# Kernel tuning notes

Hardware: AMD Instinct MI355X
Metric: run time of the kernel (lower is better)

Reference implementation:

```python
import jax, jax.numpy as jnp
import numpy as np

N_HEAD = 16
D_MODEL = 1024
D_K = D_MODEL // N_HEAD  # 64
NEG = -1000000000.0


def setup_inputs() -> dict:
    key = jax.random.key(0)
    ks = jax.random.split(key, 7)
    B, L = 4, 2048
    q = jax.random.normal(ks[0], (B, L, D_MODEL), dtype=jnp.float32)
    k = jax.random.normal(ks[1], (B, L, D_MODEL), dtype=jnp.float32)
    v = jax.random.normal(ks[2], (B, L, D_MODEL), dtype=jnp.float32)
    mask = jnp.ones((B, L, L), dtype=jnp.int32)
    s = 1.0 / np.sqrt(D_MODEL)
    w_q = jax.random.normal(ks[3], (D_MODEL, D_MODEL), dtype=jnp.float32) * s
    w_k = jax.random.normal(ks[4], (D_MODEL, D_MODEL), dtype=jnp.float32) * s
    w_v = jax.random.normal(ks[5], (D_MODEL, D_MODEL), dtype=jnp.float32) * s
    w_o = jax.random.normal(ks[6], (D_MODEL, D_MODEL), dtype=jnp.float32) * s
    return {"q": q, "k": k, "v": v, "w_q": w_q, "w_k": w_k, "w_v": w_v, "w_o": w_o, "mask": mask}


def reference(q, k, v, w_q, w_k, w_v, w_o, mask):
    B, Lq, _ = q.shape
    temperature = jnp.asarray(D_K, q.dtype) ** 0.5
    # Projections (Linear, no bias): x @ W^T, then split heads -> [B, H, L, d_k]
    qh = (q @ w_q.T).reshape(B, Lq, N_HEAD, D_K).transpose(0, 2, 1, 3)
    kh = (k @ w_k.T).reshape(B, -1, N_HEAD, D_K).transpose(0, 2, 1, 3)
    vh = (v @ w_v.T).reshape(B, -1, N_HEAD, D_K).transpose(0, 2, 1, 3)
    # Scaled dot-product attention, full [B, H, Lq, Lk] scores materialized
    attn = jnp.einsum("bhqd,bhkd->bhqk", qh / temperature, kh)
    attn = jnp.where(mask[:, None, :, :] == 0, NEG, attn)
    attn = jax.nn.softmax(attn, axis=-1)  # dropout is identity in eval mode
    out = jnp.einsum("bhqk,bhkd->bhqd", attn, vh)
    out = out.transpose(0, 2, 1, 3).reshape(B, Lq, D_MODEL)
    return out @ w_o.T
```

## Files before the change

### kernel.cpp

```cpp
#include <hip/hip_runtime.h>
#include <stdint.h>

typedef float  f32x4  __attribute__((ext_vector_type(4)));
typedef __bf16 bf16x8 __attribute__((ext_vector_type(8)));
typedef short  s16x8  __attribute__((ext_vector_type(8)));
typedef short  s16x4  __attribute__((ext_vector_type(4)));
typedef unsigned int   u32;
typedef unsigned short u16;
typedef u32 u32x2 __attribute__((ext_vector_type(2)));
typedef u32 u32x4 __attribute__((ext_vector_type(4)));

#define DM 1024
#define LQ 2048
#define NH 16

__device__ __forceinline__ u16 f2bf(float f) {
    unsigned int u = __builtin_bit_cast(unsigned int, f);
    u += 0x7FFFu + ((u >> 16) & 1u);
    return (u16)(u >> 16);
}

__device__ __forceinline__ float fexp2(float x) {
#if __has_builtin(__builtin_amdgcn_exp2f)
    return __builtin_amdgcn_exp2f(x);
#else
    return exp2f(x);
#endif
}

__device__ __forceinline__ u32 cvtpk(float lo, float hi) {
    u32 r;
    asm("v_cvt_pk_bf16_f32 %0, %1, %2" : "=v"(r) : "v"(lo), "v"(hi));
    return r;
}

__device__ __forceinline__ float max3f(float a, float b, float c) {
    float r;
    asm("v_max3_f32 %0, %1, %2, %3" : "=v"(r) : "v"(a), "v"(b), "v"(c));
    return r;
}

__device__ __forceinline__ u32 permb(u32 b, u32 a, u32 sel) {
    u32 r;
    asm("v_perm_b32 %0, %1, %2, %3" : "=v"(r) : "v"(b), "v"(a), "s"(sel));
    return r;
}

__device__ __forceinline__ f32x4 mfma32(s16x8 a, s16x8 b, f32x4 c) {
    return __builtin_amdgcn_mfma_f32_16x16x32_bf16(
        __builtin_bit_cast(bf16x8, a), __builtin_bit_cast(bf16x8, b), c, 0, 0, 0);
}

#define GLD16(gp, lp) __builtin_amdgcn_global_load_lds( \
    (__attribute__((address_space(1))) void*)(gp),      \
    (__attribute__((address_space(3))) void*)(lp), 16, 0, 0)

__global__ void k_mask_check(const int4* __restrict__ m4, int n4, int* flag) {
    bool z = false;
    for (int i = blockIdx.x * blockDim.x + threadIdx.x; i < n4;
         i += gridDim.x * blockDim.x) {
        int4 v = m4[i];
        if (v.x == 0 || v.y == 0 || v.z == 0 || v.w == 0) z = true;
    }
    if (__ballot(z)) {
        if ((threadIdx.x & 63) == 0) atomicAnd(flag, 0);
    }
}

__global__ void k_cvt_all(const float4* __restrict__ q,  const float4* __restrict__ k,
                          const float4* __restrict__ v,  const float4* __restrict__ wq,
                          const float4* __restrict__ wk, const float4* __restrict__ wv,
                          const float4* __restrict__ wo,
                          uint64_t* xq, uint64_t* xk, uint64_t* xv,
                          uint64_t* bwq, uint64_t* bwk, uint64_t* bwv, uint64_t* bwo,
                          int* flag)
{
    if (blockIdx.x == 0 && threadIdx.x == 0) *flag = 1;
    const int NX = 2097152, NW = 262144;
    const int total = 3 * NX + 4 * NW;
    const int stride = gridDim.x * blockDim.x;
    for (int idx = blockIdx.x * blockDim.x + threadIdx.x; idx < total; idx += stride) {
        const float4* s; uint64_t* d; int off;
        if (idx < 3 * NX) {
            int ji = idx >> 21;
            off = idx & (NX - 1);
            s = ji == 0 ? q : ji == 1 ? k : v;
            d = ji == 0 ? xq : ji == 1 ? xk : xv;
        } else {
            int r = idx - 3 * NX;
            int ji = r >> 18;
            off = r & (NW - 1);
            s = ji == 0 ? wq : ji == 1 ? wk : ji == 2 ? wv : wo;
            d = ji == 0 ? bwq : ji == 1 ? bwk : ji == 2 ? bwv : bwo;
        }
        float4 f = s[off];
        union { u16 u[4]; uint64_t qq; } rr;
        rr.u[0] = f2bf(f.x); rr.u[1] = f2bf(f.y);
        rr.u[2] = f2bf(f.z); rr.u[3] = f2bf(f.w);
        d[off] = rr.qq;
    }
}

template <int MODE>
__global__ __launch_bounds__(256) void k_gemm(
    const u16* __restrict__ A0, const u16* __restrict__ Bw0,
    u16* __restrict__ Cb0, float* __restrict__ Cf, float scale)
{
    constexpr int K = 1024;
    __shared__ char lA[128 * 32 * 2];
    __shared__ char lB[128 * 32 * 2];
    const int t = threadIdx.x, l = t & 63, w = t >> 6;
    const int q = l & 15, g = l >> 4;
    const int z = (MODE == 0) ? blockIdx.z : 0;
    const u16* A  = A0  + (size_t)z * 8388608;
    const u16* Bw = Bw0 + (size_t)z * 1048576;
    u16* Cb = (MODE == 0) ? Cb0 + (size_t)z * 8388608 : nullptr;
    const float scl = (MODE == 0 && z != 0) ? 1.0f : scale;
    const int lin = blockIdx.x;
    const int ytile = ((lin & 7) << 3) | ((lin >> 3) & 7);
    const int xtile = lin >> 6;
    const int m0 = ytile * 128, n0 = xtile * 128;
    const int wr = (w >> 1) * 64, wc = (w & 1) * 64;

    f32x4 acc[4][4];
#pragma unroll
    for (int i = 0; i < 4; i++)
#pragma unroll
        for (int j = 0; j < 4; j++) acc[i][j] = (f32x4){0.f, 0.f, 0.f, 0.f};

    for (int k0 = 0; k0 < K; k0 += 32) {
#pragma unroll
        for (int c = 0; c < 2; c++) {
            int i = c * 256 + t;
            int row = i >> 2, sl = i & 3;
            int ss = sl ^ (row & 3);
            GLD16(A  + (size_t)(m0 + row) * K + k0 + ss * 8, lA + (i - l) * 16);
            GLD16(Bw + (size_t)(n0 + row) * K + k0 + ss * 8, lB + (i - l) * 16);
        }
        __syncthreads();
        s16x8 af[4], bfr[4];
#pragma unroll
        for (int mt = 0; mt < 4; mt++) {
            int r = wr + mt * 16 + q;
            af[mt] = *(const s16x8*)(lA + r * 64 + ((g ^ (r & 3)) * 16));
        }
#pragma unroll
        for (int nt = 0; nt < 4; nt++) {
            int r = wc + nt * 16 + q;
            bfr[nt] = *(const s16x8*)(lB + r * 64 + ((g ^ (r & 3)) * 16));
        }
#pragma unroll
        for (int mt = 0; mt < 4; mt++)
#pragma unroll
            for (int nt = 0; nt < 4; nt++)
                acc[mt][nt] = mfma32(bfr[nt], af[mt], acc[mt][nt]);
        __syncthreads();
    }

#pragma unroll
    for (int mt = 0; mt < 4; mt++) {
        int m = m0 + wr + mt * 16 + q;
#pragma unroll
        for (int nt = 0; nt < 4; nt++) {
            int n = n0 + wc + nt * 16 + g * 4;
            f32x4 a = acc[mt][nt];
            if (MODE == 0) {
                int bb = m >> 11, row = m & 2047;
                int h = n >> 6, d = n & 63;
                s16x4 pk;
#pragma unroll
                for (int j = 0; j < 4; j++) pk[j] = (short)f2bf(a[j] * scl);
                *(s16x4*)(Cb + (((size_t)(bb * NH + h) * LQ + row) << 6) + d) = pk;
            } else {
                f32x4 o;
#pragma unroll
                for (int j = 0; j < 4; j++) o[j] = a[j] * scl;
                *(f32x4*)(Cf + (size_t)m * DM + n) = o;
            }
        }
    }
}

__global__ __launch_bounds__(256, 2) void k_attn(
    const u16* __restrict__ Qh, const u16* __restrict__ Kh,
    const u16* __restrict__ Vh, u16* __restrict__ ctx,
    const int* __restrict__ mask, const int* __restrict__ flag)
{
    __shared__ char lds[32768];
    char* lK0 = lds;
    char* lV0 = lds + 16384;
    const int t = threadIdx.x, l = t & 63, w = t >> 6;
    const int g = l >> 4, q = l & 15;
    const int p = blockIdx.x;
    const int bh = (p & 7) * 8 + ((p >> 3) >> 3);
    const int qt = ((p >> 3) & 7) * 256;
    const int allones = *flag;
    const size_t base = (size_t)bh * LQ * 64;
    const int dg = (l & 7) | ((w & 2) << 2);
    const int kg = (l >> 3) | ((w & 1) << 3);

    s16x8 qf[4][2];
#pragma unroll
    for (int qh = 0; qh < 4; qh++)
#pragma unroll
        for (int kh = 0; kh < 2; kh++)
            qf[qh][kh] = *(const s16x8*)(
                Qh + base + (size_t)(qt + w * 64 + qh * 16 + q) * 64 + kh * 32 + g * 8);

    f32x4 oacc[4][4];
#pragma unroll
    for (int qh = 0; qh < 4; qh++)
#pragma unroll
        for (int dt = 0; dt < 4; dt++) oacc[qh][dt] = (f32x4){0.f, 0.f, 0.f, 0.f};
    float mrow[4] = {-1e30f, -1e30f, -1e30f, -1e30f};
    float lrow[4] = {0.f, 0.f, 0.f, 0.f};

    auto stageK = [&](int kt, int b) {
#pragma unroll
        for (int c = 0; c < 2; c++) {
            int i = c * 256 + t;
            int row = i >> 3, sl = i & 7;
            GLD16(Kh + base + (size_t)(kt + row) * 64 + ((sl ^ (row & 7)) * 8),
                  lK0 + b * 8192 + (i - l) * 16);
        }
    };
    auto loadV = [&](int kt, s16x4* vr) {
#pragma unroll
        for (int j = 0; j < 4; j++)
            vr[j] = *(const s16x4*)(Vh + base + (size_t)(kt + kg * 4 + j) * 64 + dg * 4);
    };
    auto writeV = [&](const s16x4* vr, int b) {
        const u32 selLO = 0x05040100u, selHI = 0x07060302u;
        const int u = ((kg & 8) >> 1) | (kg & 3);
        const int bb2 = (kg >> 2) & 1;
        u32x2 vv[4];
#pragma unroll
        for (int j = 0; j < 4; j++) vv[j] = __builtin_bit_cast(u32x2, vr[j]);
#pragma unroll
        for (int jj = 0; jj < 4; jj++) {
            int d = dg * 4 + jj;
            u32 a0 = vv[0][jj >> 1], a1 = vv[1][jj >> 1];
            u32 a2 = vv[2][jj >> 1], a3 = vv[3][jj >> 1];
            u32 sel = (jj & 1) ? selHI : selLO;
            u32x2 pw = {permb(a1, a0, sel), permb(a3, a2, sel)};
            *(s16x4*)(lV0 + b * 8192 + d * 128 + ((u ^ (d & 7)) * 16) + bb2 * 8) =
                __builtin_bit_cast(s16x4, pw);
        }
    };

    {
        s16x4 vr[4];
        stageK(0, 0);
        loadV(0, vr);
        writeV(vr, 0);
    }

    int cur = 0;
    for (int kt = 0; kt < LQ; kt += 64) {
        __syncthreads();
        const bool more = (kt + 64) < LQ;
        s16x4 vr[4];
        if (more) {
            stageK(kt + 64, cur ^ 1);
            loadV(kt + 64, vr);
        }

        f32x4 sc[4][4];
#pragma unroll
        for (int qh = 0; qh < 4; qh++)
#pragma unroll
            for (int ct = 0; ct < 4; ct++) sc[qh][ct] = (f32x4){0.f, 0.f, 0.f, 0.f};
        __builtin_amdgcn_s_setprio(1);
#pragma unroll
        for (int ct = 0; ct < 4; ct++) {
            int kc = ct * 16 + q;
#pragma unroll
            for (int kh = 0; kh < 2; kh++) {
                s16x8 kf = *(const s16x8*)(lK0 + cur * 8192 + kc * 128 +
                                           (((kh * 4 + g) ^ (kc & 7)) * 16));
#pragma unroll
                for (int qh = 0; qh < 4; qh++)
                    sc[qh][ct] = mfma32(kf, qf[qh][kh], sc[qh][ct]);
            }
        }
        __builtin_amdgcn_s_setprio(0);

        if (!allones) {
            int b = bh >> 4;
#pragma unroll
            for (int qh = 0; qh < 4; qh++)
#pragma unroll
                for (int ct = 0; ct < 4; ct++)
#pragma unroll
                    for (int r = 0; r < 4; r++) {
                        int qr = qt + w * 64 + qh * 16 + q;
                        int kc = kt + ct * 16 + g * 4 + r;
                        if (mask[(size_t)(b * LQ + qr) * LQ + kc] == 0)
                            sc[qh][ct][r] = -1e9f;
                    }
        }

        float pm[4];
#pragma unroll
        for (int qh = 0; qh < 4; qh++) {
            float m0 = max3f(sc[qh][0][0], sc[qh][0][1], sc[qh][0][2]);
            m0 = max3f(m0, sc[qh][0][3], sc[qh][1][0]);
            m0 = max3f(m0, sc[qh][1][1], sc[qh][1][2]);
            m0 = max3f(m0, sc[qh][1][3], sc[qh][2][0]);
            m0 = max3f(m0, sc[qh][2][1], sc[qh][2][2]);
            m0 = max3f(m0, sc[qh][2][3], sc[qh][3][0]);
            m0 = max3f(m0, sc[qh][3][1], sc[qh][3][2]);
            m0 = fmaxf(m0, sc[qh][3][3]);
            m0 = fmaxf(m0, __shfl_xor(m0, 16, 64));
            m0 = fmaxf(m0, __shfl_xor(m0, 32, 64));
            pm[qh] = m0;
        }
        bool ok = pm[0] <= mrow[0] + 8.f;
        ok = ok && (pm[1] <= mrow[1] + 8.f);
        ok = ok && (pm[2] <= mrow[2] + 8.f);
        ok = ok && (pm[3] <= mrow[3] + 8.f);
        if (!__all(ok)) {
#pragma unroll
            for (int qh = 0; qh < 4; qh++) {
                float nm = fmaxf(mrow[qh], pm[qh]);
                float corr = fexp2(mrow[qh] - nm);
                mrow[qh] = nm;
                lrow[qh] *= corr;
                float cv[4];
#pragma unroll
                for (int r = 0; r < 4; r++) cv[r] = __shfl(corr, g * 4 + r, 64);
#pragma unroll
                for (int dt = 0; dt < 4; dt++)
#pragma unroll
                    for (int r = 0; r < 4; r++) oacc[qh][dt][r] *= cv[r];
            }
        }
        s16x8 pa32[4][2];
#pragma unroll
        for (int qh = 0; qh < 4; qh++) {
            float rs = 0.f;
#pragma unroll
            for (int ct = 0; ct < 4; ct++)
#pragma unroll
                for (int r = 0; r < 4; r++) {
                    float e = fexp2(sc[qh][ct][r] - mrow[qh]);
                    sc[qh][ct][r] = e;
                    rs += e;
                }
            rs += __shfl_xor(rs, 16, 64);
            rs += __shfl_xor(rs, 32, 64);
            lrow[qh] += rs;
#pragma unroll
            for (int s = 0; s < 2; s++) {
                u32x4 pv;
                pv.x = cvtpk(sc[qh][2 * s][0],     sc[qh][2 * s][1]);
                pv.y = cvtpk(sc[qh][2 * s][2],     sc[qh][2 * s][3]);
                pv.z = cvtpk(sc[qh][2 * s + 1][0], sc[qh][2 * s + 1][1]);
                pv.w = cvtpk(sc[qh][2 * s + 1][2], sc[qh][2 * s + 1][3]);
                pa32[qh][s] = __builtin_bit_cast(s16x8, pv);
            }
        }

        __builtin_amdgcn_s_setprio(1);
#pragma unroll
        for (int dt = 0; dt < 4; dt++) {
#pragma unroll
            for (int s = 0; s < 2; s++) {
                s16x8 vf = *(const s16x8*)(lV0 + cur * 8192 + (dt * 16 + q) * 128 +
                                           (((4 * s + g) ^ (q & 7)) * 16));
#pragma unroll
                for (int qh = 0; qh < 4; qh++)
                    oacc[qh][dt] = mfma32(pa32[qh][s], vf, oacc[qh][dt]);
            }
        }
        __builtin_amdgcn_s_setprio(0);

        if (more) writeV(vr, cur ^ 1);
        cur ^= 1;
    }

    __syncthreads();
    char* eb = lds + w * 8192;
#pragma unroll
    for (int qh = 0; qh < 4; qh++) {
        float lv[4];
#pragma unroll
        for (int r = 0; r < 4; r++) lv[r] = 1.f / __shfl(lrow[qh], g * 4 + r, 64);
#pragma unroll
        for (int dt = 0; dt < 4; dt++)
#pragma unroll
            for (int r = 0; r < 4; r++) {
                int row = qh * 16 + g * 4 + r;
                int cb = ((dt * 16 + q) * 2) ^ ((row & 7) << 4);
                *(u16*)(eb + row * 128 + cb) = f2bf(oacc[qh][dt][r] * lv[r]);
            }
    }
    __syncthreads();
    const int b = bh >> 4, h = bh & 15;
    const int token = qt + w * 64 + l;
    u16* gp = ctx + (size_t)(b * LQ + token) * DM + h * 64;
#pragma unroll
    for (int j = 0; j < 8; j++) {
        int cb = (j * 16) ^ ((l & 7) << 4);
        *(s16x8*)(gp + j * 8) = *(const s16x8*)(eb + l * 128 + cb);
    }
}

extern "C" void kernel_launch(void* const* d_in, const int* in_sizes, int n_in,
                              void* d_out, int out_size, void* d_ws, size_t ws_size,
                              hipStream_t stream)
{
    const float* q  = (const float*)d_in[0];
    const float* k  = (const float*)d_in[1];
    const float* v  = (const float*)d_in[2];
    const float* wq = (const float*)d_in[3];
    const float* wk = (const float*)d_in[4];
    const float* wv = (const float*)d_in[5];
    const float* wo = (const float*)d_in[6];
    const int* mask = (const int*)d_in[7];

    char* ws = (char*)d_ws;
    const size_t SX = (size_t)8192 * 1024 * 2;
    const size_t SW = (size_t)1024 * 1024 * 2;
    u16* xq  = (u16*)(ws);
    u16* xk  = (u16*)(ws + SX);
    u16* xv  = (u16*)(ws + 2 * SX);
    u16* bwq = (u16*)(ws + 3 * SX);
    u16* bwk = (u16*)(ws + 3 * SX + SW);
    u16* bwv = (u16*)(ws + 3 * SX + 2 * SW);
    u16* bwo = (u16*)(ws + 3 * SX + 3 * SW);
    u16* Qh  = (u16*)(ws + 3 * SX + 4 * SW);
    u16* Kh  = (u16*)(ws + 4 * SX + 4 * SW);
    u16* Vh  = (u16*)(ws + 5 * SX + 4 * SW);
    u16* ctx = (u16*)(ws + 6 * SX + 4 * SW);
    int* flag = (int*)(ws + 7 * SX + 4 * SW);

    k_cvt_all<<<2048, 256, 0, stream>>>(
        (const float4*)q, (const float4*)k, (const float4*)v,
        (const float4*)wq, (const float4*)wk, (const float4*)wv, (const float4*)wo,
        (uint64_t*)xq, (uint64_t*)xk, (uint64_t*)xv,
        (uint64_t*)bwq, (uint64_t*)bwk, (uint64_t*)bwv, (uint64_t*)bwo, flag);
    k_mask_check<<<2048, 256, 0, stream>>>((const int4*)mask,
                                           (4 * 2048 * 2048) / 4, flag);

    k_gemm<0><<<dim3(512, 1, 3), 256, 0, stream>>>(xq, bwq, Qh, nullptr,
                                                   0.18033688011112042f);

    k_attn<<<512, 256, 0, stream>>>(Qh, Kh, Vh, ctx, mask, flag);

    k_gemm<1><<<dim3(512), 256, 0, stream>>>(ctx, bwo, nullptr, (float*)d_out, 1.0f);
}
```

Before: 236.7 us.

## Fuse activation fp32-to-bf16 conversion into projection GEMM loads

Removes the standalone conversion of q/k/v activations to bf16 and instead loads fp32 tiles in the projection GEMM, converting in registers before writing to LDS. Weight conversion is merged with the mask-check pass, and the flag init becomes a memset. The softmax row-sum is restructured into vector adds. This cuts a large intermediate write/read of bf16 activations, at the cost of synchronous register-staged loads replacing async global-to-LDS loads for the A operand.

After: 239.7 us. Within noise of the previous version (+1.3%).

```diff
diff --git a/kernel.cpp b/kernel.cpp
--- a/kernel.cpp
+++ b/kernel.cpp
@@ -55,55 +55,42 @@
     (__attribute__((address_space(1))) void*)(gp),      \
     (__attribute__((address_space(3))) void*)(lp), 16, 0, 0)
 
-__global__ void k_mask_check(const int4* __restrict__ m4, int n4, int* flag) {
+__global__ void k_cvt_mask(const float4* __restrict__ wq, const float4* __restrict__ wk,
+                           const float4* __restrict__ wv, const float4* __restrict__ wo,
+                           uint64_t* bwq, uint64_t* bwk, uint64_t* bwv, uint64_t* bwo,
+                           const int4* __restrict__ m4, int* flag)
+{
+    const int NW = 262144;
+    const int totw = 4 * NW;
+    const int totm = (4 * 2048 * 2048) / 4;
+    const int stride = gridDim.x * blockDim.x;
     bool z = false;
-    for (int i = blockIdx.x * blockDim.x + threadIdx.x; i < n4;
-         i += gridDim.x * blockDim.x) {
-        int4 v = m4[i];
-        if (v.x == 0 || v.y == 0 || v.z == 0 || v.w == 0) z = true;
+    for (int idx = blockIdx.x * blockDim.x + threadIdx.x; idx < totw + totm;
+         idx += stride) {
+        if (idx < totw) {
+            int ji = idx >> 18, off = idx & (NW - 1);
+            const float4* s = ji == 0 ? wq : ji == 1 ? wk : ji == 2 ? wv : wo;
+            uint64_t* d = ji == 0 ? bwq : ji == 1 ? bwk : ji == 2 ? bwv : bwo;
+            float4 f = s[off];
+            union { u16 u[4]; uint64_t qq; } rr;
+            rr.u[0] = f2bf(f.x); rr.u[1] = f2bf(f.y);
+            rr.u[2] = f2bf(f.z); rr.u[3] = f2bf(f.w);
+            d[off] = rr.qq;
+        } else {
+            int4 v = m4[idx - totw];
+            if (v.x == 0 || v.y == 0 || v.z == 0 || v.w == 0) z = true;
+        }
     }
     if (__ballot(z)) {
         if ((threadIdx.x & 63) == 0) atomicAnd(flag, 0);
     }
 }
 
-__global__ void k_cvt_all(const float4* __restrict__ q,  const float4* __restrict__ k,
-                          const float4* __restrict__ v,  const float4* __restrict__ wq,
-                          const float4* __restrict__ wk, const float4* __restrict__ wv,
-                          const float4* __restrict__ wo,
-                          uint64_t* xq, uint64_t* xk, uint64_t* xv,
-                          uint64_t* bwq, uint64_t* bwk, uint64_t* bwv, uint64_t* bwo,
-                          int* flag)
-{
-    if (blockIdx.x == 0 && threadIdx.x == 0) *flag = 1;
-    const int NX = 2097152, NW = 262144;
-    const int total = 3 * NX + 4 * NW;
-    const int stride = gridDim.x * blockDim.x;
-    for (int idx = blockIdx.x * blockDim.x + threadIdx.x; idx < total; idx += stride) {
-        const float4* s; uint64_t* d; int off;
-        if (idx < 3 * NX) {
-            int ji = idx >> 21;
-            off = idx & (NX - 1);
-            s = ji == 0 ? q : ji == 1 ? k : v;
-            d = ji == 0 ? xq : ji == 1 ? xk : xv;
-        } else {
-            int r = idx - 3 * NX;
-            int ji = r >> 18;
-            off = r & (NW - 1);
-            s = ji == 0 ? wq : ji == 1 ? wk : ji == 2 ? wv : wo;
-            d = ji == 0 ? bwq : ji == 1 ? bwk : ji == 2 ? bwv : bwo;
-        }
-        float4 f = s[off];
-        union { u16 u[4]; uint64_t qq; } rr;
-        rr.u[0] = f2bf(f.x); rr.u[1] = f2bf(f.y);
-        rr.u[2] = f2bf(f.z); rr.u[3] = f2bf(f.w);
-        d[off] = rr.qq;
-    }
-}
-
 template <int MODE>
 __global__ __launch_bounds__(256) void k_gemm(
-    const u16* __restrict__ A0, const u16* __restrict__ Bw0,
+    const float* __restrict__ Aq, const float* __restrict__ Ak,
+    const float* __restrict__ Av, const u16* __restrict__ Ab,
+    const u16* __restrict__ Bw0,
     u16* __restrict__ Cb0, float* __restrict__ Cf, float scale)
 {
     constexpr int K = 1024;
@@ -112,7 +99,7 @@
     const int t = threadIdx.x, l = t & 63, w = t >> 6;
     const int q = l & 15, g = l >> 4;
     const int z = (MODE == 0) ? blockIdx.z : 0;
-    const u16* A  = A0  + (size_t)z * 8388608;
+    const float* Af = (MODE == 0) ? (z == 0 ? Aq : (z == 1 ? Ak : Av)) : nullptr;
     const u16* Bw = Bw0 + (size_t)z * 1048576;
     u16* Cb = (MODE == 0) ? Cb0 + (size_t)z * 8388608 : nullptr;
     const float scl = (MODE == 0 && z != 0) ? 1.0f : scale;
@@ -129,13 +116,40 @@
         for (int j = 0; j < 4; j++) acc[i][j] = (f32x4){0.f, 0.f, 0.f, 0.f};
 
     for (int k0 = 0; k0 < K; k0 += 32) {
-#pragma unroll
-        for (int c = 0; c < 2; c++) {
-            int i = c * 256 + t;
-            int row = i >> 2, sl = i & 3;
-            int ss = sl ^ (row & 3);
-            GLD16(A  + (size_t)(m0 + row) * K + k0 + ss * 8, lA + (i - l) * 16);
-            GLD16(Bw + (size_t)(n0 + row) * K + k0 + ss * 8, lB + (i - l) * 16);
+        if (MODE == 0) {
+            float4 f0[2], f1[2];
+#pragma unroll
+            for (int c = 0; c < 2; c++) {
+                int i = c * 256 + t;
+                int row = i >> 2, sl = i & 3;
+                int ss = sl ^ (row & 3);
+                const float* ap = Af + (size_t)(m0 + row) * K + k0 + ss * 8;
+                f0[c] = *(const float4*)ap;
+                f1[c] = *(const float4*)(ap + 4);
+            }
+#pragma unroll
+            for (int c = 0; c < 2; c++) {
+                int i = c * 256 + t;
+                int row = i >> 2, sl = i & 3;
+                int ss = sl ^ (row & 3);
+                GLD16(Bw + (size_t)(n0 + row) * K + k0 + ss * 8, lB + (i - l) * 16);
+            }
+#pragma unroll
+            for (int c = 0; c < 2; c++) {
+                int i = c * 256 + t;
+                u32x4 pk = {cvtpk(f0[c].x, f0[c].y), cvtpk(f0[c].z, f0[c].w),
+                            cvtpk(f1[c].x, f1[c].y), cvtpk(f1[c].z, f1[c].w)};
+                *(u32x4*)(lA + i * 16) = pk;
+            }
+        } else {
+#pragma unroll
+            for (int c = 0; c < 2; c++) {
+                int i = c * 256 + t;
+                int row = i >> 2, sl = i & 3;
+                int ss = sl ^ (row & 3);
+                GLD16(Ab + (size_t)(m0 + row) * K + k0 + ss * 8, lA + (i - l) * 16);
+                GLD16(Bw + (size_t)(n0 + row) * K + k0 + ss * 8, lB + (i - l) * 16);
+            }
         }
         __syncthreads();
         s16x8 af[4], bfr[4];
@@ -338,15 +352,13 @@
         s16x8 pa32[4][2];
 #pragma unroll
         for (int qh = 0; qh < 4; qh++) {
-            float rs = 0.f;
 #pragma unroll
             for (int ct = 0; ct < 4; ct++)
 #pragma unroll
-                for (int r = 0; r < 4; r++) {
-                    float e = fexp2(sc[qh][ct][r] - mrow[qh]);
-                    sc[qh][ct][r] = e;
-                    rs += e;
-                }
+                for (int r = 0; r < 4; r++)
+                    sc[qh][ct][r] = fexp2(sc[qh][ct][r] - mrow[qh]);
+            f32x4 vs = (sc[qh][0] + sc[qh][1]) + (sc[qh][2] + sc[qh][3]);
+            float rs = (vs[0] + vs[1]) + (vs[2] + vs[3]);
             rs += __shfl_xor(rs, 16, 64);
             rs += __shfl_xor(rs, 32, 64);
             lrow[qh] += rs;
@@ -422,9 +434,6 @@
     char* ws = (char*)d_ws;
     const size_t SX = (size_t)8192 * 1024 * 2;
     const size_t SW = (size_t)1024 * 1024 * 2;
-    u16* xq  = (u16*)(ws);
-    u16* xk  = (u16*)(ws + SX);
-    u16* xv  = (u16*)(ws + 2 * SX);
     u16* bwq = (u16*)(ws + 3 * SX);
     u16* bwk = (u16*)(ws + 3 * SX + SW);
     u16* bwv = (u16*)(ws + 3 * SX + 2 * SW);
@@ -435,18 +444,17 @@
     u16* ctx = (u16*)(ws + 6 * SX + 4 * SW);
     int* flag = (int*)(ws + 7 * SX + 4 * SW);
 
-    k_cvt_all<<<2048, 256, 0, stream>>>(
-        (const float4*)q, (const float4*)k, (const float4*)v,
+    hipMemsetAsync(flag, 0xFF, 4, stream);
+    k_cvt_mask<<<2048, 256, 0, stream>>>(
         (const float4*)wq, (const float4*)wk, (const float4*)wv, (const float4*)wo,
-        (uint64_t*)xq, (uint64_t*)xk, (uint64_t*)xv,
-        (uint64_t*)bwq, (uint64_t*)bwk, (uint64_t*)bwv, (uint64_t*)bwo, flag);
-    k_mask_check<<<2048, 256, 0, stream>>>((const int4*)mask,
-                                           (4 * 2048 * 2048) / 4, flag);
-
-    k_gemm<0><<<dim3(512, 1, 3), 256, 0, stream>>>(xq, bwq, Qh, nullptr,
-                                                   0.18033688011112042f);
+        (uint64_t*)bwq, (uint64_t*)bwk, (uint64_t*)bwv, (uint64_t*)bwo,
+        (const int4*)mask, flag);
+
+    k_gemm<0><<<dim3(512, 1, 3), 256, 0, stream>>>(
+        q, k, v, nullptr, bwq, Qh, nullptr, 0.18033688011112042f);
 
     k_attn<<<512, 256, 0, stream>>>(Qh, Kh, Vh, ctx, mask, flag);
 
-    k_gemm<1><<<dim3(512), 256, 0, stream>>>(ctx, bwo, nullptr, (float*)d_out, 1.0f);
-}
+    k_gemm<1><<<dim3(512), 256, 0, stream>>>(
+        nullptr, nullptr, nullptr, ctx, bwo, nullptr, (float*)d_out, 1.0f);
+}
```
